# Performance work log

Hardware: AMD Instinct MI355X
Metric: run time of the kernel (lower is better)

## Reference

```python
import jax, jax.numpy as jnp
import numpy as np

# static config (levels=4, CDA=False branch -> self_attn_4, scale=4, f=False)
SHAPES = [(80, 80), (40, 40), (20, 20), (10, 10)]
D = 256; NH = 8; NL = 4; NP = 4; DFF = 1024; DH = D // NH
L = sum(h * w for h, w in SHAPES)  # 8500
B = 1


def layer_norm(x, g, b, eps=1e-5):
    m = jnp.mean(x, axis=-1, keepdims=True)
    v = jnp.mean((x - m) ** 2, axis=-1, keepdims=True)
    return (x - m) * jax.lax.rsqrt(v + eps) * g + b


def ms_deform_attn_core(value, loc, attn):
    # value: [B, L, NH, DH]; loc: [B, Lq, NH, NL, NP, 2] in [0,1]; attn: [B, Lq, NH, NL, NP]
    Bq, Lq = loc.shape[0], loc.shape[1]
    out = jnp.zeros((Bq, NH, Lq, DH), value.dtype)
    start = 0
    for lvl, (Hl, Wl) in enumerate(SHAPES):
        v = value[:, start:start + Hl * Wl]          # [B, HW, NH, DH]
        start += Hl * Wl
        v = v.transpose(0, 2, 1, 3)                  # [B, NH, HW, DH]
        ll = loc[:, :, :, lvl]                       # [B, Lq, NH, NP, 2]
        # grid_sample semantics: align_corners=False, padding_mode='zeros'
        x = ll[..., 0] * Wl - 0.5
        y = ll[..., 1] * Hl - 0.5
        x0 = jnp.floor(x); y0 = jnp.floor(y)
        acc = jnp.zeros((Bq, NH, Lq, NP, DH), value.dtype)
        for dy in (0, 1):
            for dx in (0, 1):
                xi = x0 + dx; yi = y0 + dy
                w = (1.0 - jnp.abs(x - xi)) * (1.0 - jnp.abs(y - yi))  # [B,Lq,NH,NP]
                valid = (xi >= 0) & (xi < Wl) & (yi >= 0) & (yi < Hl)
                xi_c = jnp.clip(xi, 0, Wl - 1).astype(jnp.int32)
                yi_c = jnp.clip(yi, 0, Hl - 1).astype(jnp.int32)
                lin = (yi_c * Wl + xi_c).transpose(0, 2, 1, 3).reshape(Bq, NH, Lq * NP)
                g = jnp.take_along_axis(v, lin[..., None], axis=2).reshape(Bq, NH, Lq, NP, DH)
                wv = (w * valid.astype(w.dtype)).transpose(0, 2, 1, 3)[..., None]
                acc = acc + g * wv
        aw = attn[:, :, :, lvl].transpose(0, 2, 1, 3)[..., None]  # [B,NH,Lq,NP,1]
        out = out + jnp.sum(acc * aw, axis=3)
    return out.transpose(0, 2, 1, 3).reshape(Bq, Lq, NH * DH)


def setup_inputs():
    key = jax.random.key(0)
    ks = jax.random.split(key, 24)
    s = 0.02
    d = {}
    d['src'] = jax.random.normal(ks[0], (B, L, D), jnp.float32)
    d['pos'] = jax.random.normal(ks[1], (B, L, D), jnp.float32)
    d['reference_points'] = jax.random.uniform(ks[2], (B, L, NL, 2), jnp.float32)
    d['spatial_shapes'] = jnp.array(SHAPES, jnp.int32)
    d['level_start_index'] = jnp.array(np.cumsum([0] + [h * w for h, w in SHAPES[:-1]]), jnp.int32)
    d['scale'] = 4
    # MSDeformAttn params
    d['Wo'] = jax.random.normal(ks[3], (D, NH * NL * NP * 2), jnp.float32) * s
    d['bo'] = jax.random.normal(ks[4], (NH * NL * NP * 2,), jnp.float32) * s
    d['Wa'] = jax.random.normal(ks[5], (D, NH * NL * NP), jnp.float32) * s
    d['ba'] = jax.random.normal(ks[6], (NH * NL * NP,), jnp.float32) * s
    d['Wv'] = jax.random.normal(ks[7], (D, D), jnp.float32) * s
    d['bv'] = jnp.zeros((D,), jnp.float32)
    d['Wout'] = jax.random.normal(ks[8], (D, D), jnp.float32) * s
    d['bout'] = jnp.zeros((D,), jnp.float32)
    # FFN + LayerNorms
    d['W1'] = jax.random.normal(ks[9], (D, DFF), jnp.float32) * s
    d['b1'] = jnp.zeros((DFF,), jnp.float32)
    d['W2'] = jax.random.normal(ks[10], (DFF, D), jnp.float32) * s
    d['b2'] = jnp.zeros((D,), jnp.float32)
    d['g1'] = jnp.ones((D,), jnp.float32); d['be1'] = jnp.zeros((D,), jnp.float32)
    d['g2'] = jnp.ones((D,), jnp.float32); d['be2'] = jnp.zeros((D,), jnp.float32)
    return d


def reference(src, pos, reference_points, spatial_shapes, level_start_index, scale,
              Wo, bo, Wa, ba, Wv, bv, Wout, bout, W1, b1, W2, b2, g1, be1, g2, be2):
    Bq, Lq, _ = src.shape
    q = src + pos  # with_pos_embed
    # sampling offsets & attention weights (softmax over levels*points)
    off = (q @ Wo + bo).reshape(Bq, Lq, NH, NL, NP, 2)
    attn = jax.nn.softmax((q @ Wa + ba).reshape(Bq, Lq, NH, NL * NP), axis=-1)
    attn = attn.reshape(Bq, Lq, NH, NL, NP)
    value = (src @ Wv + bv).reshape(Bq, L, NH, DH)
    # offset normalizer is (W, H) per level
    normalizer = jnp.stack([spatial_shapes[:, 1], spatial_shapes[:, 0]], -1).astype(src.dtype)
    loc = reference_points[:, :, None, :, None, :] + off / normalizer[None, None, None, :, None, :]
    src2 = ms_deform_attn_core(value, loc, attn) @ Wout + bout
    # residual + norm1 (dropout = eval identity)
    x = layer_norm(src + src2, g1, be1)
    # FFN
    ffn = jax.nn.relu(x @ W1 + b1) @ W2 + b2
    x = layer_norm(x + ffn, g2, be2)
    return x
```

## Files before the change

kernel.cpp:

```cpp
#include <hip/hip_runtime.h>
#include <hip/hip_bf16.h>
#include <string.h>

#define D 256
#define NH 8
#define DH 32
#define NL 4
#define NP 4
#define DFF 1024
#define LTOT 8500

typedef __bf16 bf16x8 __attribute__((ext_vector_type(8)));
typedef float floatx4 __attribute__((ext_vector_type(4)));

__device__ inline unsigned bpack(float a, float b) {
    __hip_bfloat16 ha = __float2bfloat16(a), hb = __float2bfloat16(b);
    unsigned short ua, ub;
    memcpy(&ua, &ha, 2); memcpy(&ub, &hb, 2);
    return (unsigned)ua | ((unsigned)ub << 16);
}

__device__ inline void gload16(const void* g, void* l) {
    __builtin_amdgcn_global_load_lds((const __attribute__((address_space(1))) void*)g,
                                     (__attribute__((address_space(3))) void*)l,
                                     16, 0, 0);
}

__global__ void transpose_all(const float* W0, const float* W1_, const float* W2_,
                              const float* W3, const float* W4, const float* W5,
                              __hip_bfloat16* T0, __hip_bfloat16* T1, __hip_bfloat16* T2,
                              __hip_bfloat16* T3, __hip_bfloat16* T4, __hip_bfloat16* T5,
                              const float* src, const float* pos,
                              __hip_bfloat16* qb, __hip_bfloat16* srcb) {
    int id = blockIdx.x;
    if (id >= 736) {
        int idx = (id - 736) * 2048 + threadIdx.x * 8;
        if (idx < LTOT * 256) {
            float4 s0 = *(const float4*)(src + idx);
            float4 s1 = *(const float4*)(src + idx + 4);
            float4 p0 = *(const float4*)(pos + idx);
            float4 p1 = *(const float4*)(pos + idx + 4);
            uint4 us, uq;
            us.x = bpack(s0.x, s0.y); us.y = bpack(s0.z, s0.w);
            us.z = bpack(s1.x, s1.y); us.w = bpack(s1.z, s1.w);
            uq.x = bpack(s0.x + p0.x, s0.y + p0.y); uq.y = bpack(s0.z + p0.z, s0.w + p0.w);
            uq.z = bpack(s1.x + p1.x, s1.y + p1.y); uq.w = bpack(s1.z + p1.z, s1.w + p1.w);
            *(uint4*)(srcb + idx) = us;
            *(uint4*)(qb + idx)  = uq;
        }
        return;
    }
    const int cum[7] = {0, 64, 96, 160, 224, 480, 736};
    int mi = 0;
    while (id >= cum[mi + 1]) mi++;
    int lid = id - cum[mi];
    const float* W; __hip_bfloat16* T; int K, N;
    switch (mi) {
        case 0: W = W0; T = T0; K = 256;  N = 256;  break;
        case 1: W = W1_; T = T1; K = 256; N = 128;  break;
        case 2: W = W2_; T = T2; K = 256; N = 256;  break;
        case 3: W = W3; T = T3; K = 256;  N = 256;  break;
        case 4: W = W4; T = T4; K = 256;  N = 1024; break;
        default: W = W5; T = T5; K = 1024; N = 256; break;
    }
    int ntx = N >> 5;
    int n0 = (lid % ntx) * 32, k0 = (lid / ntx) * 32;
    __shared__ float t[32][33];
    int tx = threadIdx.x & 31, ty = threadIdx.x >> 5;
#pragma unroll
    for (int i = 0; i < 32; i += 8)
        t[ty + i][tx] = W[(size_t)(k0 + ty + i) * N + n0 + tx];
    __syncthreads();
#pragma unroll
    for (int i = 0; i < 32; i += 8)
        T[(size_t)(n0 + ty + i) * K + k0 + tx] = __float2bfloat16(t[tx][ty + i]);
}

__global__ __launch_bounds__(256) void gemm97(
    const __hip_bfloat16* __restrict__ A, const __hip_bfloat16* __restrict__ BT,
    const float* __restrict__ bias, float* __restrict__ Cf, __hip_bfloat16* __restrict__ Cb,
    int M, int N, int K, int relu) {
    constexpr int BM = 128, BN = 128, BK = 32;
    __shared__ __align__(16) __hip_bfloat16 sA[BM * BK];
    __shared__ __align__(16) __hip_bfloat16 sB[BN * BK];

    int tid = threadIdx.x, wave = tid >> 6, lane = tid & 63;
    int m0 = blockIdx.y * BM, n0 = blockIdx.x * BN;
    int wm = (wave >> 1) * 64, wn = (wave & 1) * 64;

    floatx4 acc[4][4];
#pragma unroll
    for (int i = 0; i < 4; i++)
#pragma unroll
        for (int j = 0; j < 4; j++)
#pragma unroll
            for (int e = 0; e < 4; e++) acc[i][j][e] = 0.f;

    int l4r = lane >> 2;
    int l4c = (lane & 3) * 8;
    int lrow = lane & 15, lk = (lane >> 4) * 8;

    int grA[2];
#pragma unroll
    for (int i = 0; i < 2; i++) {
        int g = m0 + wave * 32 + i * 16 + l4r;
        if (g >= M) g = M - 1;
        grA[i] = g;
    }

    for (int k0 = 0; k0 < K; k0 += BK) {
#pragma unroll
        for (int i = 0; i < 2; i++)
            gload16(A + (size_t)grA[i] * K + k0 + l4c,
                    (char*)sA + wave * 2048 + i * 1024);
#pragma unroll
        for (int i = 0; i < 2; i++)
            gload16(BT + (size_t)(n0 + wave * 32 + i * 16 + l4r) * K + k0 + l4c,
                    (char*)sB + wave * 2048 + i * 1024);
        __syncthreads();

        bf16x8 af[4], bfr[4];
#pragma unroll
        for (int tm = 0; tm < 4; tm++)
            af[tm] = *(const bf16x8*)(&sA[(wm + tm * 16 + lrow) * BK + lk]);
#pragma unroll
        for (int tn = 0; tn < 4; tn++)
            bfr[tn] = *(const bf16x8*)(&sB[(wn + tn * 16 + lrow) * BK + lk]);
#pragma unroll
        for (int tm = 0; tm < 4; tm++)
#pragma unroll
            for (int tn = 0; tn < 4; tn++)
                acc[tm][tn] = __builtin_amdgcn_mfma_f32_16x16x32_bf16(af[tm], bfr[tn], acc[tm][tn], 0, 0, 0);
        __syncthreads();
    }

    int lcol = lane & 15, lr4 = (lane >> 4) * 4;
#pragma unroll
    for (int tm = 0; tm < 4; tm++) {
#pragma unroll
        for (int i = 0; i < 4; i++) {
            int row = m0 + wm + tm * 16 + lr4 + i;
            if (row < M) {
#pragma unroll
                for (int tn = 0; tn < 4; tn++) {
                    int col = n0 + wn + tn * 16 + lcol;
                    float v = acc[tm][tn][i] + bias[col];
                    if (relu) v = fmaxf(v, 0.f);
                    if (Cf) Cf[(size_t)row * N + col] = v;
                    if (Cb) Cb[(size_t)row * N + col] = __float2bfloat16(v);
                }
            }
        }
    }
}

__global__ __launch_bounds__(256) void proj2(
    const __hip_bfloat16* __restrict__ qb, const __hip_bfloat16* __restrict__ srcb,
    const __hip_bfloat16* __restrict__ WoT, const __hip_bfloat16* __restrict__ WaT,
    const __hip_bfloat16* __restrict__ WvT,
    const float* __restrict__ bo, const float* __restrict__ ba, const float* __restrict__ bv,
    float* __restrict__ locb, float* __restrict__ attnb, __hip_bfloat16* __restrict__ valb,
    int M) {
    constexpr int BM = 128, BN = 128, BK = 32, K = 256;
    __shared__ __align__(16) __hip_bfloat16 sA[BM * BK];
    __shared__ __align__(16) __hip_bfloat16 sB[BN * BK];

    int n0 = blockIdx.x * BN;
    int m0 = blockIdx.y * BM;

    const __hip_bfloat16* BT;
    const __hip_bfloat16* A;
    const float* bias;
    int ncol0, Nout;
    float* Cf; __hip_bfloat16* Cb;
    if (n0 < 256)      { A = qb;   BT = WoT; bias = bo; ncol0 = n0;       Nout = 256; Cf = locb;  Cb = nullptr; }
    else if (n0 < 384) { A = qb;   BT = WaT; bias = ba; ncol0 = 0;        Nout = 128; Cf = attnb; Cb = nullptr; }
    else               { A = srcb; BT = WvT; bias = bv; ncol0 = n0 - 384; Nout = 256; Cf = nullptr; Cb = valb; }

    int tid = threadIdx.x, wave = tid >> 6, lane = tid & 63;
    int wm = (wave >> 1) * 64, wn = (wave & 1) * 64;

    floatx4 acc[4][4];
#pragma unroll
    for (int i = 0; i < 4; i++)
#pragma unroll
        for (int j = 0; j < 4; j++)
#pragma unroll
            for (int e = 0; e < 4; e++) acc[i][j][e] = 0.f;

    int l4r = lane >> 2, l4c = (lane & 3) * 8;
    int lrow = lane & 15, lk = (lane >> 4) * 8;

    int grA[2];
#pragma unroll
    for (int i = 0; i < 2; i++) {
        int g = m0 + wave * 32 + i * 16 + l4r;
        if (g >= M) g = M - 1;
        grA[i] = g;
    }

    for (int k0 = 0; k0 < K; k0 += BK) {
#pragma unroll
        for (int i = 0; i < 2; i++)
            gload16(A + (size_t)grA[i] * K + k0 + l4c,
                    (char*)sA + wave * 2048 + i * 1024);
#pragma unroll
        for (int i = 0; i < 2; i++)
            gload16(BT + (size_t)(ncol0 + wave * 32 + i * 16 + l4r) * K + k0 + l4c,
                    (char*)sB + wave * 2048 + i * 1024);
        __syncthreads();

        bf16x8 af[4], bfr[4];
#pragma unroll
        for (int tm = 0; tm < 4; tm++)
            af[tm] = *(const bf16x8*)(&sA[(wm + tm * 16 + lrow) * BK + lk]);
#pragma unroll
        for (int tn = 0; tn < 4; tn++)
            bfr[tn] = *(const bf16x8*)(&sB[(wn + tn * 16 + lrow) * BK + lk]);
#pragma unroll
        for (int tm = 0; tm < 4; tm++)
#pragma unroll
            for (int tn = 0; tn < 4; tn++)
                acc[tm][tn] = __builtin_amdgcn_mfma_f32_16x16x32_bf16(af[tm], bfr[tn], acc[tm][tn], 0, 0, 0);
        __syncthreads();
    }

    int lcol = lane & 15, lr4 = (lane >> 4) * 4;
#pragma unroll
    for (int tm = 0; tm < 4; tm++) {
#pragma unroll
        for (int i = 0; i < 4; i++) {
            int row = m0 + wm + tm * 16 + lr4 + i;
            if (row < M) {
#pragma unroll
                for (int tn = 0; tn < 4; tn++) {
                    int col = ncol0 + wn + tn * 16 + lcol;
                    float v = acc[tm][tn][i] + bias[col];
                    if (Cf) Cf[(size_t)row * Nout + col] = v;
                    else    Cb[(size_t)row * Nout + col] = __float2bfloat16(v);
                }
            }
        }
    }
}

__global__ __launch_bounds__(256) void deform(const __hip_bfloat16* __restrict__ value,
                                              const float* __restrict__ locraw,
                                              const float* __restrict__ logits,
                                              const float* __restrict__ refp,
                                              __hip_bfloat16* __restrict__ out) {
    __shared__ float wS[4][8][16][4];
    __shared__ int   aS[4][8][16][4];
    int tid = threadIdx.x;
    int q0 = blockIdx.x * 4;

    {
        int sub = tid >> 6, h = (tid >> 3) & 7, t8 = tid & 7;
        int q = q0 + sub;
        const float* lg = logits + q * 128 + h * 16;
        float l0 = lg[t8], l1 = lg[t8 + 8];
        float mx = fmaxf(l0, l1);
#pragma unroll
        for (int m = 1; m < 8; m <<= 1) mx = fmaxf(mx, __shfl_xor(mx, m, 64));
        float e0 = __expf(l0 - mx), e1 = __expf(l1 - mx);
        float s = e0 + e1;
#pragma unroll
        for (int m = 1; m < 8; m <<= 1) s += __shfl_xor(s, m, 64);
        float inv = 1.f / s;

        const int starts[4] = {0, 6400, 8000, 8400};
#pragma unroll
        for (int j = 0; j < 2; j++) {
            int pp = t8 + 8 * j;
            float a = (j ? e1 : e0) * inv;
            int l = pp >> 2;
            int Wl = 80 >> l;
            float nv = (float)Wl;
            float rx = refp[q * 8 + l * 2 + 0];
            float ry = refp[q * 8 + l * 2 + 1];
            float lx = rx + locraw[q * 256 + h * 32 + pp * 2 + 0] / nv;
            float ly = ry + locraw[q * 256 + h * 32 + pp * 2 + 1] / nv;
            float x = lx * nv - 0.5f;
            float y = ly * nv - 0.5f;
            float x0f = floorf(x), y0f = floorf(y);
            float fx = x - x0f, fy = y - y0f;
            int x0 = (int)x0f, y0 = (int)y0f;
            float wts[4] = {(1.f - fx) * (1.f - fy), fx * (1.f - fy),
                            (1.f - fx) * fy,         fx * fy};
            int st = starts[l];
#pragma unroll
            for (int t = 0; t < 4; t++) {
                int xi = x0 + (t & 1), yi = y0 + (t >> 1);
                bool valid = (xi >= 0) & (xi < Wl) & (yi >= 0) & (yi < Wl);
                int xc = min(max(xi, 0), Wl - 1), yc = min(max(yi, 0), Wl - 1);
                wS[sub][h][pp][t] = valid ? wts[t] * a : 0.f;
                aS[sub][h][pp][t] = (st + yc * Wl + xc) * 512 + h * 64;
            }
        }
    }
    __syncthreads();

    int sub = tid >> 6, h = (tid >> 3) & 7, l8 = tid & 7;
    int q = q0 + sub;
    const char* vb = (const char*)value;
    int lo = l8 * 8;
    float a0 = 0.f, a1 = 0.f, a2 = 0.f, a3 = 0.f;
#pragma unroll
    for (int p = 0; p < 16; p++) {
        floatx4 w = *(const floatx4*)&wS[sub][h][p][0];
        int4 av = *(const int4*)&aS[sub][h][p][0];
#pragma unroll
        for (int t = 0; t < 4; t++) {
            int ad = (t == 0) ? av.x : (t == 1) ? av.y : (t == 2) ? av.z : av.w;
            uint2 u = *(const uint2*)(vb + ad + lo);
            float wt = w[t];
            a0 += wt * __uint_as_float(u.x << 16);
            a1 += wt * __uint_as_float(u.x & 0xffff0000u);
            a2 += wt * __uint_as_float(u.y << 16);
            a3 += wt * __uint_as_float(u.y & 0xffff0000u);
        }
    }
    uint2 o;
    o.x = bpack(a0, a1);
    o.y = bpack(a2, a3);
    *(uint2*)((char*)out + q * 512 + h * 64 + l8 * 8) = o;
}

__global__ __launch_bounds__(512) void gemm_ln(
    const __hip_bfloat16* __restrict__ A, const __hip_bfloat16* __restrict__ BT,
    const float* __restrict__ bias, const float* __restrict__ resid,
    const float* __restrict__ g, const float* __restrict__ be,
    float* __restrict__ outf, __hip_bfloat16* __restrict__ outb,
    int M, int K) {
    constexpr int BM = 32, BK = 32;
    __shared__ __align__(16) __hip_bfloat16 sA[BM * BK];
    __shared__ __align__(16) __hip_bfloat16 sB[256 * BK];
    __shared__ float psum[8][32], psq[8][32], mS[32], rS[32];

    int tid = threadIdx.x;
    int wave = tid >> 6, lane = tid & 63;
    int m0 = blockIdx.x * BM;

    floatx4 acc[2][2];
#pragma unroll
    for (int i = 0; i < 2; i++)
#pragma unroll
        for (int j = 0; j < 2; j++)
#pragma unroll
            for (int e = 0; e < 4; e++) acc[i][j][e] = 0.f;

    int l4r = lane >> 2, l4c = (lane & 3) * 8;
    int lrow = lane & 15, lk = (lane >> 4) * 8;

    int grA = m0 + wave * 16 + l4r;
    if (grA >= M) grA = M - 1;

    for (int k0 = 0; k0 < K; k0 += BK) {
        if (wave < 2)
            gload16(A + (size_t)grA * K + k0 + l4c, (char*)sA + wave * 1024);
#pragma unroll
        for (int i = 0; i < 2; i++)
            gload16(BT + (size_t)(wave * 32 + i * 16 + l4r) * K + k0 + l4c,
                    (char*)sB + wave * 2048 + i * 1024);
        __syncthreads();

        bf16x8 af[2], bfr[2];
#pragma unroll
        for (int tm = 0; tm < 2; tm++)
            af[tm] = *(const bf16x8*)(&sA[(tm * 16 + lrow) * BK + lk]);
#pragma unroll
        for (int tn = 0; tn < 2; tn++)
            bfr[tn] = *(const bf16x8*)(&sB[(wave * 32 + tn * 16 + lrow) * BK + lk]);
#pragma unroll
        for (int tm = 0; tm < 2; tm++)
#pragma unroll
            for (int tn = 0; tn < 2; tn++)
                acc[tm][tn] = __builtin_amdgcn_mfma_f32_16x16x32_bf16(af[tm], bfr[tn], acc[tm][tn], 0, 0, 0);
        __syncthreads();
    }

    int lcol = lane & 15, quad = lane >> 4;
    float v[2][2][4];
#pragma unroll
    for (int tm = 0; tm < 2; tm++) {
#pragma unroll
        for (int i = 0; i < 4; i++) {
            int row = tm * 16 + quad * 4 + i;
            int grow = m0 + row; if (grow >= M) grow = M - 1;
#pragma unroll
            for (int tn = 0; tn < 2; tn++) {
                int col = wave * 32 + tn * 16 + lcol;
                v[tm][tn][i] = acc[tm][tn][i] + bias[col] + resid[(size_t)grow * 256 + col];
            }
        }
    }

#pragma unroll
    for (int tm = 0; tm < 2; tm++) {
#pragma unroll
        for (int i = 0; i < 4; i++) {
            float s = 0.f, s2 = 0.f;
#pragma unroll
            for (int tn = 0; tn < 2; tn++) { float x = v[tm][tn][i]; s += x; s2 += x * x; }
#pragma unroll
            for (int m = 1; m < 16; m <<= 1) {
                s  += __shfl_xor(s, m, 64);
                s2 += __shfl_xor(s2, m, 64);
            }
            if (lcol == 0) {
                int row = tm * 16 + quad * 4 + i;
                psum[wave][row] = s;
                psq[wave][row]  = s2;
            }
        }
    }
    __syncthreads();
    if (tid < 32) {
        float s = 0.f, s2 = 0.f;
#pragma unroll
        for (int w = 0; w < 8; w++) { s += psum[w][tid]; s2 += psq[w][tid]; }
        float m = s * (1.f / 256.f);
        float var = fmaxf(s2 * (1.f / 256.f) - m * m, 0.f);
        mS[tid] = m;
        rS[tid] = rsqrtf(var + 1e-5f);
    }
    __syncthreads();

#pragma unroll
    for (int tm = 0; tm < 2; tm++) {
#pragma unroll
        for (int i = 0; i < 4; i++) {
            int row = tm * 16 + quad * 4 + i;
            int grow = m0 + row;
            if (grow < M) {
                float m = mS[row], r = rS[row];
#pragma unroll
                for (int tn = 0; tn < 2; tn++) {
                    int col = wave * 32 + tn * 16 + lcol;
                    float o = (v[tm][tn][i] - m) * r * g[col] + be[col];
                    outf[(size_t)grow * 256 + col] = o;
                    if (outb) outb[(size_t)grow * 256 + col] = __float2bfloat16(o);
                }
            }
        }
    }
}

extern "C" void kernel_launch(void* const* d_in, const int* in_sizes, int n_in,
                              void* d_out, int out_size, void* d_ws, size_t ws_size,
                              hipStream_t stream) {
    const float* src  = (const float*)d_in[0];
    const float* pos  = (const float*)d_in[1];
    const float* refp = (const float*)d_in[2];
    const float* Wo   = (const float*)d_in[6];
    const float* bo   = (const float*)d_in[7];
    const float* Wa   = (const float*)d_in[8];
    const float* ba   = (const float*)d_in[9];
    const float* Wv   = (const float*)d_in[10];
    const float* bv   = (const float*)d_in[11];
    const float* Wout = (const float*)d_in[12];
    const float* bout = (const float*)d_in[13];
    const float* W1   = (const float*)d_in[14];
    const float* b1   = (const float*)d_in[15];
    const float* W2   = (const float*)d_in[16];
    const float* b2   = (const float*)d_in[17];
    const float* g1   = (const float*)d_in[18];
    const float* be1  = (const float*)d_in[19];
    const float* g2   = (const float*)d_in[20];
    const float* be2  = (const float*)d_in[21];
    float* out = (float*)d_out;
    char* ws = (char*)d_ws;

    __hip_bfloat16* WoT   = (__hip_bfloat16*)(ws + 0);
    __hip_bfloat16* WaT   = (__hip_bfloat16*)(ws + 131072);
    __hip_bfloat16* WvT   = (__hip_bfloat16*)(ws + 196608);
    __hip_bfloat16* WoutT = (__hip_bfloat16*)(ws + 327680);
    __hip_bfloat16* W1T   = (__hip_bfloat16*)(ws + 458752);
    __hip_bfloat16* W2T   = (__hip_bfloat16*)(ws + 983040);
    float*          locb  = (float*)(ws + 1507328);
    float*          attnb = (float*)(ws + 10211328);
    __hip_bfloat16* valb  = (__hip_bfloat16*)(ws + 14563328);
    __hip_bfloat16* aob   = (__hip_bfloat16*)(ws + 18915328);
    float*          x1    = (float*)(ws + 23267328);
    __hip_bfloat16* x1b   = (__hip_bfloat16*)(ws + 31971328);
    __hip_bfloat16* hb    = (__hip_bfloat16*)(ws + 36323328);
    __hip_bfloat16* qb    = (__hip_bfloat16*)(ws + 36323328);
    __hip_bfloat16* srcb  = (__hip_bfloat16*)(ws + 36323328 + 4352000);

    transpose_all<<<736 + 1063, 256, 0, stream>>>(Wo, Wa, Wv, Wout, W1, W2,
                                                  WoT, WaT, WvT, WoutT, W1T, W2T,
                                                  src, pos, qb, srcb);

    proj2<<<dim3(5, 67), 256, 0, stream>>>(qb, srcb, WoT, WaT, WvT, bo, ba, bv,
                                           locb, attnb, valb, LTOT);

    deform<<<2125, 256, 0, stream>>>(valb, locb, attnb, refp, aob);

    gemm_ln<<<266, 512, 0, stream>>>(aob, WoutT, bout, src, g1, be1, x1, x1b, LTOT, 256);

    gemm97<<<dim3(8, 67), 256, 0, stream>>>(x1b, W1T, b1, nullptr, hb, LTOT, 1024, 256, 1);

    gemm_ln<<<266, 512, 0, stream>>>(hb, W2T, b2, x1, g2, be2, out, nullptr, LTOT, 1024);
}
```

Baseline: 212.7 us.

## Shrink GEMM tiles, deepen K-step to 64, and XOR-swizzle LDS layout

All GEMM kernels (proj2, the FFN GEMM, and both GEMM+LayerNorm kernels) move to smaller output tiles (64x64, or 16 rows for the LN GEMMs) with a K-step of 64. LDS tiles get an XOR-swizzled column layout to avoid bank conflicts on the fragment reads. Grids double or quadruple so more blocks fill the MI355X's CUs for M=8500. The cost is less data reuse per block, more redundant weight loads in gemm_ln (the full 256-column B tile is loaded for only 16 rows), and more launch-level blocks. The proj2 attention-weight column offset is also made consistent with the new tile width.

```diff
diff --git a/kernel.cpp b/kernel.cpp
--- a/kernel.cpp
+++ b/kernel.cpp
@@ -76,73 +76,74 @@
         T[(size_t)(n0 + ty + i) * K + k0 + tx] = __float2bfloat16(t[tx][ty + i]);
 }
 
-__global__ __launch_bounds__(256) void gemm97(
+__global__ __launch_bounds__(256) void gemm_t(
     const __hip_bfloat16* __restrict__ A, const __hip_bfloat16* __restrict__ BT,
     const float* __restrict__ bias, float* __restrict__ Cf, __hip_bfloat16* __restrict__ Cb,
     int M, int N, int K, int relu) {
-    constexpr int BM = 128, BN = 128, BK = 32;
+    constexpr int BM = 64, BN = 64, BK = 64;
     __shared__ __align__(16) __hip_bfloat16 sA[BM * BK];
     __shared__ __align__(16) __hip_bfloat16 sB[BN * BK];
 
     int tid = threadIdx.x, wave = tid >> 6, lane = tid & 63;
     int m0 = blockIdx.y * BM, n0 = blockIdx.x * BN;
-    int wm = (wave >> 1) * 64, wn = (wave & 1) * 64;
-
-    floatx4 acc[4][4];
-#pragma unroll
-    for (int i = 0; i < 4; i++)
-#pragma unroll
-        for (int j = 0; j < 4; j++)
+    int wm = (wave >> 1) * 32, wn = (wave & 1) * 32;
+
+    floatx4 acc[2][2];
+#pragma unroll
+    for (int i = 0; i < 2; i++)
+#pragma unroll
+        for (int j = 0; j < 2; j++)
 #pragma unroll
             for (int e = 0; e < 4; e++) acc[i][j][e] = 0.f;
 
-    int l4r = lane >> 2;
-    int l4c = (lane & 3) * 8;
-    int lrow = lane & 15, lk = (lane >> 4) * 8;
-
-    int grA[2];
+    int lrow = lane & 15, swz = lrow & 7;
+    int scol = ((lane & 7) ^ (lane >> 3)) << 3;
+
+    const __hip_bfloat16* aP[2];
+    const __hip_bfloat16* bP[2];
 #pragma unroll
     for (int i = 0; i < 2; i++) {
-        int g = m0 + wave * 32 + i * 16 + l4r;
-        if (g >= M) g = M - 1;
-        grA[i] = g;
-    }
+        int ra = m0 + i * 32 + wave * 8 + (lane >> 3); if (ra >= M) ra = M - 1;
+        aP[i] = A + (size_t)ra * K + scol;
+        int rb = n0 + i * 32 + wave * 8 + (lane >> 3);
+        bP[i] = BT + (size_t)rb * K + scol;
+    }
+    int dOff = wave * 1024 + lane * 16;
 
     for (int k0 = 0; k0 < K; k0 += BK) {
 #pragma unroll
-        for (int i = 0; i < 2; i++)
-            gload16(A + (size_t)grA[i] * K + k0 + l4c,
-                    (char*)sA + wave * 2048 + i * 1024);
-#pragma unroll
-        for (int i = 0; i < 2; i++)
-            gload16(BT + (size_t)(n0 + wave * 32 + i * 16 + l4r) * K + k0 + l4c,
-                    (char*)sB + wave * 2048 + i * 1024);
-        __syncthreads();
-
-        bf16x8 af[4], bfr[4];
-#pragma unroll
-        for (int tm = 0; tm < 4; tm++)
-            af[tm] = *(const bf16x8*)(&sA[(wm + tm * 16 + lrow) * BK + lk]);
-#pragma unroll
-        for (int tn = 0; tn < 4; tn++)
-            bfr[tn] = *(const bf16x8*)(&sB[(wn + tn * 16 + lrow) * BK + lk]);
-#pragma unroll
-        for (int tm = 0; tm < 4; tm++)
-#pragma unroll
-            for (int tn = 0; tn < 4; tn++)
-                acc[tm][tn] = __builtin_amdgcn_mfma_f32_16x16x32_bf16(af[tm], bfr[tn], acc[tm][tn], 0, 0, 0);
+        for (int i = 0; i < 2; i++) gload16(aP[i] + k0, (char*)sA + i * 4096 + dOff);
+#pragma unroll
+        for (int i = 0; i < 2; i++) gload16(bP[i] + k0, (char*)sB + i * 4096 + dOff);
+        __syncthreads();
+#pragma unroll
+        for (int kk = 0; kk < 2; kk++) {
+            int co = (((kk << 2) + (lane >> 4)) ^ swz) << 3;
+            bf16x8 af[2], bfr[2];
+#pragma unroll
+            for (int tm = 0; tm < 2; tm++)
+                af[tm] = *(const bf16x8*)(&sA[(wm + tm * 16 + lrow) * BK + co]);
+#pragma unroll
+            for (int tn = 0; tn < 2; tn++)
+                bfr[tn] = *(const bf16x8*)(&sB[(wn + tn * 16 + lrow) * BK + co]);
+#pragma unroll
+            for (int tm = 0; tm < 2; tm++)
+#pragma unroll
+                for (int tn = 0; tn < 2; tn++)
+                    acc[tm][tn] = __builtin_amdgcn_mfma_f32_16x16x32_bf16(af[tm], bfr[tn], acc[tm][tn], 0, 0, 0);
+        }
         __syncthreads();
     }
 
     int lcol = lane & 15, lr4 = (lane >> 4) * 4;
 #pragma unroll
-    for (int tm = 0; tm < 4; tm++) {
+    for (int tm = 0; tm < 2; tm++) {
 #pragma unroll
         for (int i = 0; i < 4; i++) {
             int row = m0 + wm + tm * 16 + lr4 + i;
             if (row < M) {
 #pragma unroll
-                for (int tn = 0; tn < 4; tn++) {
+                for (int tn = 0; tn < 2; tn++) {
                     int col = n0 + wn + tn * 16 + lcol;
                     float v = acc[tm][tn][i] + bias[col];
                     if (relu) v = fmaxf(v, 0.f);
@@ -161,7 +162,7 @@
     const float* __restrict__ bo, const float* __restrict__ ba, const float* __restrict__ bv,
     float* __restrict__ locb, float* __restrict__ attnb, __hip_bfloat16* __restrict__ valb,
     int M) {
-    constexpr int BM = 128, BN = 128, BK = 32, K = 256;
+    constexpr int BM = 64, BN = 64, BK = 64, K = 256;
     __shared__ __align__(16) __hip_bfloat16 sA[BM * BK];
     __shared__ __align__(16) __hip_bfloat16 sB[BN * BK];
 
@@ -174,66 +175,68 @@
     int ncol0, Nout;
     float* Cf; __hip_bfloat16* Cb;
     if (n0 < 256)      { A = qb;   BT = WoT; bias = bo; ncol0 = n0;       Nout = 256; Cf = locb;  Cb = nullptr; }
-    else if (n0 < 384) { A = qb;   BT = WaT; bias = ba; ncol0 = 0;        Nout = 128; Cf = attnb; Cb = nullptr; }
+    else if (n0 < 384) { A = qb;   BT = WaT; bias = ba; ncol0 = n0 - 256; Nout = 128; Cf = attnb; Cb = nullptr; }
     else               { A = srcb; BT = WvT; bias = bv; ncol0 = n0 - 384; Nout = 256; Cf = nullptr; Cb = valb; }
 
     int tid = threadIdx.x, wave = tid >> 6, lane = tid & 63;
-    int wm = (wave >> 1) * 64, wn = (wave & 1) * 64;
-
-    floatx4 acc[4][4];
-#pragma unroll
-    for (int i = 0; i < 4; i++)
-#pragma unroll
-        for (int j = 0; j < 4; j++)
+    int wm = (wave >> 1) * 32, wn = (wave & 1) * 32;
+
+    floatx4 acc[2][2];
+#pragma unroll
+    for (int i = 0; i < 2; i++)
+#pragma unroll
+        for (int j = 0; j < 2; j++)
 #pragma unroll
             for (int e = 0; e < 4; e++) acc[i][j][e] = 0.f;
 
-    int l4r = lane >> 2, l4c = (lane & 3) * 8;
-    int lrow = lane & 15, lk = (lane >> 4) * 8;
-
-    int grA[2];
+    int lrow = lane & 15, swz = lrow & 7;
+    int scol = ((lane & 7) ^ (lane >> 3)) << 3;
+
+    const __hip_bfloat16* aP[2];
+    const __hip_bfloat16* bP[2];
 #pragma unroll
     for (int i = 0; i < 2; i++) {
-        int g = m0 + wave * 32 + i * 16 + l4r;
-        if (g >= M) g = M - 1;
-        grA[i] = g;
-    }
+        int ra = m0 + i * 32 + wave * 8 + (lane >> 3); if (ra >= M) ra = M - 1;
+        aP[i] = A + (size_t)ra * K + scol;
+        int rb = ncol0 + i * 32 + wave * 8 + (lane >> 3);
+        bP[i] = BT + (size_t)rb * K + scol;
+    }
+    int dOff = wave * 1024 + lane * 16;
 
     for (int k0 = 0; k0 < K; k0 += BK) {
 #pragma unroll
-        for (int i = 0; i < 2; i++)
-            gload16(A + (size_t)grA[i] * K + k0 + l4c,
-                    (char*)sA + wave * 2048 + i * 1024);
-#pragma unroll
-        for (int i = 0; i < 2; i++)
-            gload16(BT + (size_t)(ncol0 + wave * 32 + i * 16 + l4r) * K + k0 + l4c,
-                    (char*)sB + wave * 2048 + i * 1024);
-        __syncthreads();
-
-        bf16x8 af[4], bfr[4];
-#pragma unroll
-        for (int tm = 0; tm < 4; tm++)
-            af[tm] = *(const bf16x8*)(&sA[(wm + tm * 16 + lrow) * BK + lk]);
-#pragma unroll
-        for (int tn = 0; tn < 4; tn++)
-            bfr[tn] = *(const bf16x8*)(&sB[(wn + tn * 16 + lrow) * BK + lk]);
-#pragma unroll
-        for (int tm = 0; tm < 4; tm++)
-#pragma unroll
-            for (int tn = 0; tn < 4; tn++)
-                acc[tm][tn] = __builtin_amdgcn_mfma_f32_16x16x32_bf16(af[tm], bfr[tn], acc[tm][tn], 0, 0, 0);
+        for (int i = 0; i < 2; i++) gload16(aP[i] + k0, (char*)sA + i * 4096 + dOff);
+#pragma unroll
+        for (int i = 0; i < 2; i++) gload16(bP[i] + k0, (char*)sB + i * 4096 + dOff);
+        __syncthreads();
+#pragma unroll
+        for (int kk = 0; kk < 2; kk++) {
+            int co = (((kk << 2) + (lane >> 4)) ^ swz) << 3;
+            bf16x8 af[2], bfr[2];
+#pragma unroll
+            for (int tm = 0; tm < 2; tm++)
+                af[tm] = *(const bf16x8*)(&sA[(wm + tm * 16 + lrow) * BK + co]);
+#pragma unroll
+            for (int tn = 0; tn < 2; tn++)
+                bfr[tn] = *(const bf16x8*)(&sB[(wn + tn * 16 + lrow) * BK + co]);
+#pragma unroll
+            for (int tm = 0; tm < 2; tm++)
+#pragma unroll
+                for (int tn = 0; tn < 2; tn++)
+                    acc[tm][tn] = __builtin_amdgcn_mfma_f32_16x16x32_bf16(af[tm], bfr[tn], acc[tm][tn], 0, 0, 0);
+        }
         __syncthreads();
     }
 
     int lcol = lane & 15, lr4 = (lane >> 4) * 4;
 #pragma unroll
-    for (int tm = 0; tm < 4; tm++) {
+    for (int tm = 0; tm < 2; tm++) {
 #pragma unroll
         for (int i = 0; i < 4; i++) {
             int row = m0 + wm + tm * 16 + lr4 + i;
             if (row < M) {
 #pragma unroll
-                for (int tn = 0; tn < 4; tn++) {
+                for (int tn = 0; tn < 2; tn++) {
                     int col = ncol0 + wn + tn * 16 + lcol;
                     float v = acc[tm][tn][i] + bias[col];
                     if (Cf) Cf[(size_t)row * Nout + col] = v;
@@ -332,90 +335,84 @@
     const float* __restrict__ g, const float* __restrict__ be,
     float* __restrict__ outf, __hip_bfloat16* __restrict__ outb,
     int M, int K) {
-    constexpr int BM = 32, BK = 32;
+    constexpr int BM = 16, BK = 64;
     __shared__ __align__(16) __hip_bfloat16 sA[BM * BK];
     __shared__ __align__(16) __hip_bfloat16 sB[256 * BK];
-    __shared__ float psum[8][32], psq[8][32], mS[32], rS[32];
+    __shared__ float psum[8][16], psq[8][16], mS[16], rS[16];
 
     int tid = threadIdx.x;
     int wave = tid >> 6, lane = tid & 63;
     int m0 = blockIdx.x * BM;
 
-    floatx4 acc[2][2];
-#pragma unroll
-    for (int i = 0; i < 2; i++)
-#pragma unroll
-        for (int j = 0; j < 2; j++)
-#pragma unroll
-            for (int e = 0; e < 4; e++) acc[i][j][e] = 0.f;
-
-    int l4r = lane >> 2, l4c = (lane & 3) * 8;
-    int lrow = lane & 15, lk = (lane >> 4) * 8;
-
-    int grA = m0 + wave * 16 + l4r;
-    if (grA >= M) grA = M - 1;
+    floatx4 acc[2];
+#pragma unroll
+    for (int j = 0; j < 2; j++)
+#pragma unroll
+        for (int e = 0; e < 4; e++) acc[j][e] = 0.f;
+
+    int lrow = lane & 15, swz = lrow & 7;
+
+    int scolA = ((lane & 7) ^ (lane >> 3)) << 3;
+    int grA = m0 + wave * 8 + (lane >> 3); if (grA >= M) grA = M - 1;
+    const __hip_bfloat16* aP = A + (size_t)grA * K + scolA;
+
+    int scolB = ((tid & 7) ^ ((tid >> 3) & 7)) << 3;
+    const __hip_bfloat16* bP[4];
+#pragma unroll
+    for (int i = 0; i < 4; i++)
+        bP[i] = BT + (size_t)(i * 64 + (tid >> 3)) * K + scolB;
 
     for (int k0 = 0; k0 < K; k0 += BK) {
-        if (wave < 2)
-            gload16(A + (size_t)grA * K + k0 + l4c, (char*)sA + wave * 1024);
-#pragma unroll
-        for (int i = 0; i < 2; i++)
-            gload16(BT + (size_t)(wave * 32 + i * 16 + l4r) * K + k0 + l4c,
-                    (char*)sB + wave * 2048 + i * 1024);
-        __syncthreads();
-
-        bf16x8 af[2], bfr[2];
-#pragma unroll
-        for (int tm = 0; tm < 2; tm++)
-            af[tm] = *(const bf16x8*)(&sA[(tm * 16 + lrow) * BK + lk]);
-#pragma unroll
-        for (int tn = 0; tn < 2; tn++)
-            bfr[tn] = *(const bf16x8*)(&sB[(wave * 32 + tn * 16 + lrow) * BK + lk]);
-#pragma unroll
-        for (int tm = 0; tm < 2; tm++)
+        if (wave < 2) gload16(aP + k0, (char*)sA + wave * 1024 + lane * 16);
+#pragma unroll
+        for (int i = 0; i < 4; i++) gload16(bP[i] + k0, (char*)sB + i * 8192 + tid * 16);
+        __syncthreads();
+#pragma unroll
+        for (int kk = 0; kk < 2; kk++) {
+            int co = (((kk << 2) + (lane >> 4)) ^ swz) << 3;
+            bf16x8 af, bfr[2];
+            af = *(const bf16x8*)(&sA[lrow * BK + co]);
 #pragma unroll
             for (int tn = 0; tn < 2; tn++)
-                acc[tm][tn] = __builtin_amdgcn_mfma_f32_16x16x32_bf16(af[tm], bfr[tn], acc[tm][tn], 0, 0, 0);
+                bfr[tn] = *(const bf16x8*)(&sB[(wave * 32 + tn * 16 + lrow) * BK + co]);
+#pragma unroll
+            for (int tn = 0; tn < 2; tn++)
+                acc[tn] = __builtin_amdgcn_mfma_f32_16x16x32_bf16(af, bfr[tn], acc[tn], 0, 0, 0);
+        }
         __syncthreads();
     }
 
     int lcol = lane & 15, quad = lane >> 4;
-    float v[2][2][4];
-#pragma unroll
-    for (int tm = 0; tm < 2; tm++) {
-#pragma unroll
-        for (int i = 0; i < 4; i++) {
-            int row = tm * 16 + quad * 4 + i;
-            int grow = m0 + row; if (grow >= M) grow = M - 1;
-#pragma unroll
-            for (int tn = 0; tn < 2; tn++) {
-                int col = wave * 32 + tn * 16 + lcol;
-                v[tm][tn][i] = acc[tm][tn][i] + bias[col] + resid[(size_t)grow * 256 + col];
-            }
-        }
-    }
-
-#pragma unroll
-    for (int tm = 0; tm < 2; tm++) {
-#pragma unroll
-        for (int i = 0; i < 4; i++) {
-            float s = 0.f, s2 = 0.f;
-#pragma unroll
-            for (int tn = 0; tn < 2; tn++) { float x = v[tm][tn][i]; s += x; s2 += x * x; }
-#pragma unroll
-            for (int m = 1; m < 16; m <<= 1) {
-                s  += __shfl_xor(s, m, 64);
-                s2 += __shfl_xor(s2, m, 64);
-            }
-            if (lcol == 0) {
-                int row = tm * 16 + quad * 4 + i;
-                psum[wave][row] = s;
-                psq[wave][row]  = s2;
-            }
+    float v[2][4];
+#pragma unroll
+    for (int i = 0; i < 4; i++) {
+        int row = quad * 4 + i;
+        int grow = m0 + row; if (grow >= M) grow = M - 1;
+#pragma unroll
+        for (int tn = 0; tn < 2; tn++) {
+            int col = wave * 32 + tn * 16 + lcol;
+            v[tn][i] = acc[tn][i] + bias[col] + resid[(size_t)grow * 256 + col];
+        }
+    }
+
+#pragma unroll
+    for (int i = 0; i < 4; i++) {
+        float s = 0.f, s2 = 0.f;
+#pragma unroll
+        for (int tn = 0; tn < 2; tn++) { float x = v[tn][i]; s += x; s2 += x * x; }
+#pragma unroll
+        for (int m = 1; m < 16; m <<= 1) {
+            s  += __shfl_xor(s, m, 64);
+            s2 += __shfl_xor(s2, m, 64);
+        }
+        if (lcol == 0) {
+            int row = quad * 4 + i;
+            psum[wave][row] = s;
+            psq[wave][row]  = s2;
         }
     }
     __syncthreads();
-    if (tid < 32) {
+    if (tid < 16) {
         float s = 0.f, s2 = 0.f;
 #pragma unroll
         for (int w = 0; w < 8; w++) { s += psum[w][tid]; s2 += psq[w][tid]; }
@@ -427,20 +424,17 @@
     __syncthreads();
 
 #pragma unroll
-    for (int tm = 0; tm < 2; tm++) {
-#pragma unroll
-        for (int i = 0; i < 4; i++) {
-            int row = tm * 16 + quad * 4 + i;
-            int grow = m0 + row;
-            if (grow < M) {
-                float m = mS[row], r = rS[row];
-#pragma unroll
-                for (int tn = 0; tn < 2; tn++) {
-                    int col = wave * 32 + tn * 16 + lcol;
-                    float o = (v[tm][tn][i] - m) * r * g[col] + be[col];
-                    outf[(size_t)grow * 256 + col] = o;
-                    if (outb) outb[(size_t)grow * 256 + col] = __float2bfloat16(o);
-                }
+    for (int i = 0; i < 4; i++) {
+        int row = quad * 4 + i;
+        int grow = m0 + row;
+        if (grow < M) {
+            float m = mS[row], r = rS[row];
+#pragma unroll
+            for (int tn = 0; tn < 2; tn++) {
+                int col = wave * 32 + tn * 16 + lcol;
+                float o = (v[tn][i] - m) * r * g[col] + be[col];
+                outf[(size_t)grow * 256 + col] = o;
+                if (outb) outb[(size_t)grow * 256 + col] = __float2bfloat16(o);
             }
         }
     }
@@ -491,14 +485,14 @@
                                                   WoT, WaT, WvT, WoutT, W1T, W2T,
                                                   src, pos, qb, srcb);
 
-    proj2<<<dim3(5, 67), 256, 0, stream>>>(qb, srcb, WoT, WaT, WvT, bo, ba, bv,
-                                           locb, attnb, valb, LTOT);
+    proj2<<<dim3(10, 133), 256, 0, stream>>>(qb, srcb, WoT, WaT, WvT, bo, ba, bv,
+                                             locb, attnb, valb, LTOT);
 
     deform<<<2125, 256, 0, stream>>>(valb, locb, attnb, refp, aob);
 
-    gemm_ln<<<266, 512, 0, stream>>>(aob, WoutT, bout, src, g1, be1, x1, x1b, LTOT, 256);
-
-    gemm97<<<dim3(8, 67), 256, 0, stream>>>(x1b, W1T, b1, nullptr, hb, LTOT, 1024, 256, 1);
-
-    gemm_ln<<<266, 512, 0, stream>>>(hb, W2T, b2, x1, g2, be2, out, nullptr, LTOT, 1024);
-}
+    gemm_ln<<<532, 512, 0, stream>>>(aob, WoutT, bout, src, g1, be1, x1, x1b, LTOT, 256);
+
+    gemm_t<<<dim3(16, 133), 256, 0, stream>>>(x1b, W1T, b1, nullptr, hb, LTOT, 1024, 256, 1);
+
+    gemm_ln<<<532, 512, 0, stream>>>(hb, W2T, b2, x1, g2, be2, out, nullptr, LTOT, 1024);
+}
```

Result: faster. 197.0 us (-7.4%).
